# Performance work log

Hardware: AMD Instinct MI355X
Metric: run time of the kernel (lower is better)

The kernel has to match this reference:

```python
import jax, jax.numpy as jnp
import numpy as np

RMS_EPS = 1e-8
Q_EPS = 1e-5

def rms_norm(x):
    # RMSNorm without learnable scale, as in BitNet reference BitLinear
    return x * jax.lax.rsqrt(jnp.mean(x * x, axis=-1, keepdims=True) + RMS_EPS)

def activation_quant(x):
    # per-token absmax int8 quant/dequant
    scale = 127.0 / jnp.clip(jnp.max(jnp.abs(x), axis=-1, keepdims=True), Q_EPS)
    return jnp.clip(jnp.round(x * scale), -128, 127) / scale

def weight_quant(w):
    # ternary absmean quant/dequant
    scale = 1.0 / jnp.clip(jnp.mean(jnp.abs(w)), Q_EPS)
    return jnp.clip(jnp.round(w * scale), -1, 1) / scale

def bitlinear(x, w):
    # forward path of BitLinear: RMSNorm -> quantized matmul (STE is identity in fwd)
    xn = rms_norm(x)
    xq = xn + jax.lax.stop_gradient(activation_quant(xn) - xn)
    wq = w + jax.lax.stop_gradient(weight_quant(w) - w)
    return jnp.einsum('bsh,oh->bso', xq, wq)

def setup_inputs() -> dict:
    key = jax.random.key(0)
    k1, k2, k3 = jax.random.split(key, 3)
    H, I = 2048, 8192  # hidden_size, intermediate_size = 4*H
    x = jax.random.normal(k1, (4, 2048, H), jnp.float32)
    w_gate = jax.random.normal(k2, (2 * I, H), jnp.float32) * 0.02
    w_down = jax.random.normal(k3, (H, I), jnp.float32) * 0.02
    return {"x": x, "w_gate": w_gate, "w_down": w_down}

def reference(x, w_gate, w_down):
    y = bitlinear(x, w_gate)          # [B,S,2I]
    gate, v = jnp.split(y, 2, axis=-1)
    return bitlinear(jax.nn.silu(gate) * v, w_down)  # [B,S,H]
```

## Files before the change

### kernel.cpp

```cpp
#include <hip/hip_runtime.h>


using char8  = __attribute__((ext_vector_type(8))) signed char;
using int4v  = __attribute__((ext_vector_type(4))) int;
using half8  = __attribute__((ext_vector_type(8))) _Float16;

__device__ __forceinline__ void glds16(const void* g, void* l) {
  __builtin_amdgcn_global_load_lds((const __attribute__((address_space(1))) void*)g,
                                   (__attribute__((address_space(3))) void*)l, 16, 0, 0);
}

__global__ __launch_bounds__(256) void reduce_abs_kernel(
    const float4* __restrict__ w, float* __restrict__ partials, int n4) {
  int t = threadIdx.x;
  int gid = blockIdx.x * 256 + t;
  int stride = gridDim.x * 256;
  float s = 0.f;
  for (int i = gid; i < n4; i += stride) {
    float4 u = w[i];
    s += fabsf(u.x) + fabsf(u.y) + fabsf(u.z) + fabsf(u.w);
  }
  __shared__ float sm[256];
  sm[t] = s; __syncthreads();
  for (int off = 128; off > 0; off >>= 1) {
    if (t < off) sm[t] += sm[t + off];
    __syncthreads();
  }
  if (t == 0) partials[blockIdx.x] = sm[0];
}

__global__ __launch_bounds__(256) void finalize_kernel(
    const float* __restrict__ pf, float* __restrict__ scales) {
  __shared__ float sm[256];
  int t = threadIdx.x;
  float s = pf[t] + pf[t + 256] + pf[t + 512] + pf[t + 768];
  sm[t] = s; __syncthreads();
  for (int off = 128; off > 0; off >>= 1) {
    if (t < off) sm[t] += sm[t + off];
    __syncthreads();
  }
  if (t == 0) {
    float c = fmaxf(sm[0] / 33554432.0f, 1e-5f);
    scales[0] = c; scales[2] = 1.0f / c;
  }
  __syncthreads();
  s = pf[1024 + t] + pf[1280 + t] + pf[1536 + t] + pf[1792 + t];
  sm[t] = s; __syncthreads();
  for (int off = 128; off > 0; off >>= 1) {
    if (t < off) sm[t] += sm[t + off];
    __syncthreads();
  }
  if (t == 0) {
    float c = fmaxf(sm[0] / 16777216.0f, 1e-5f);
    scales[1] = c; scales[3] = 1.0f / c;
  }
}

__global__ __launch_bounds__(256) void quant_weight_kernel(
    const float4* __restrict__ w, char8* __restrict__ wq,
    const float* __restrict__ invp, int n8) {
  float inv = *invp;
  int stride = gridDim.x * 256;
  for (int i = blockIdx.x * 256 + threadIdx.x; i < n8; i += stride) {
    float4 a = w[2 * i], b = w[2 * i + 1];
    float v[8] = {a.x, a.y, a.z, a.w, b.x, b.y, b.z, b.w};
    char8 o;
#pragma unroll
    for (int j = 0; j < 8; ++j) {
      float q = rintf(v[j] * inv);
      q = fminf(fmaxf(q, -1.f), 1.f);
      o[j] = (signed char)(int)q;
    }
    wq[i] = o;
  }
}

__global__ __launch_bounds__(256) void act_quant_f32_kernel(
    const float* __restrict__ in, signed char* __restrict__ out,
    float* __restrict__ fscale) {
  const int token = blockIdx.x, t = threadIdx.x;
  const float4* row = (const float4*)(in + (size_t)token * 2048);
  float4 a = row[2 * t], b = row[2 * t + 1];
  float v[8] = {a.x, a.y, a.z, a.w, b.x, b.y, b.z, b.w};
  float ss = 0.f, am = 0.f;
#pragma unroll
  for (int j = 0; j < 8; ++j) { ss += v[j] * v[j]; am = fmaxf(am, fabsf(v[j])); }
  __shared__ float s1[256], s2[256];
  s1[t] = ss; s2[t] = am; __syncthreads();
  for (int off = 128; off > 0; off >>= 1) {
    if (t < off) { s1[t] += s1[t + off]; s2[t] = fmaxf(s2[t], s2[t + off]); }
    __syncthreads();
  }
  float r = 1.0f / sqrtf(s1[0] * (1.0f / 2048.0f) + 1e-8f);
  float f = fmaxf(s2[0] * r, 1e-5f);
  float s = 127.0f / f;
  if (t == 0) fscale[token] = f * (1.0f / 127.0f);
  char8 o;
#pragma unroll
  for (int j = 0; j < 8; ++j) {
    float q = rintf((v[j] * r) * s);
    q = fminf(fmaxf(q, -128.f), 127.f);
    o[j] = (signed char)(int)q;
  }
  ((char8*)(out + (size_t)token * 2048))[t] = o;
}

__global__ __launch_bounds__(256) void act_quant_h_kernel(
    const _Float16* __restrict__ in, signed char* __restrict__ out,
    float* __restrict__ fscale) {
  const int token = blockIdx.x, t = threadIdx.x;
  const half8* row = (const half8*)(in + (size_t)token * 8192);
  float v[32];
  float ss = 0.f, am = 0.f;
#pragma unroll
  for (int c = 0; c < 4; ++c) {
    half8 u = row[c * 256 + t];
#pragma unroll
    for (int j = 0; j < 8; ++j) {
      float f = (float)u[j]; v[c * 8 + j] = f;
      ss += f * f; am = fmaxf(am, fabsf(f));
    }
  }
  __shared__ float s1[256], s2[256];
  s1[t] = ss; s2[t] = am; __syncthreads();
  for (int off = 128; off > 0; off >>= 1) {
    if (t < off) { s1[t] += s1[t + off]; s2[t] = fmaxf(s2[t], s2[t + off]); }
    __syncthreads();
  }
  float r = 1.0f / sqrtf(s1[0] * (1.0f / 8192.0f) + 1e-8f);
  float f = fmaxf(s2[0] * r, 1e-5f);
  float s = 127.0f / f;
  if (t == 0) fscale[token] = f * (1.0f / 127.0f);
#pragma unroll
  for (int c = 0; c < 4; ++c) {
    char8 o;
#pragma unroll
    for (int j = 0; j < 8; ++j) {
      float q = rintf((v[c * 8 + j] * r) * s);
      q = fminf(fmaxf(q, -128.f), 127.f);
      o[j] = (signed char)(int)q;
    }
    ((char8*)(out + (size_t)token * 8192))[c * 256 + t] = o;
  }
}

__global__ __launch_bounds__(256, 2) void gemm1_kernel(
    const signed char* __restrict__ A,
    const signed char* __restrict__ B,
    const float* __restrict__ f1, const float* __restrict__ cgp,
    _Float16* __restrict__ Z) {
  constexpr int K = 2048, I = 8192, NT = K / 64;
  constexpr int BUF = 24576;
  __shared__ __align__(16) signed char Ls[3 * BUF];
  const int t0 = blockIdx.y * 128, n0 = blockIdx.x * 128;
  const int tid = threadIdx.x, w = tid >> 6, l = tid & 63;
  const int wm = (w >> 1) * 64, wn = (w & 1) * 64;
  const int lrow = l & 15, lchunk = (l >> 4) * 16;

  int4v ag[4][4], av[4][4];
#pragma unroll
  for (int i = 0; i < 4; ++i)
#pragma unroll
    for (int j = 0; j < 4; ++j) { ag[i][j] = {0,0,0,0}; av[i][j] = {0,0,0,0}; }

  const signed char* src[6];
  int dst[6];
#pragma unroll
  for (int r = 0; r < 6; ++r) {
    int u = w * 6 + r;
    if (u < 8) {
      src[r] = A + (size_t)(t0 + u * 16 + lrow) * K + lchunk;
      dst[r] = u * 1024;
    } else {
      int v = u - 8;
      int grow = (v < 8) ? (n0 + v * 16 + lrow) : (I + n0 + (v - 8) * 16 + lrow);
      src[r] = B + (size_t)grow * K + lchunk;
      dst[r] = 8192 + v * 1024;
    }
  }

#pragma unroll
  for (int p = 0; p < 3; ++p)
#pragma unroll
    for (int r = 0; r < 6; ++r) glds16(src[r] + p * 64, &Ls[p * BUF + dst[r]]);
  asm volatile("s_waitcnt vmcnt(12)" ::: "memory");
  __builtin_amdgcn_s_barrier();
  __builtin_amdgcn_sched_barrier(0);

  const int aoff = (wm >> 4) * 1024 + l * 16;
  const int goff = 8192 + (wn >> 4) * 1024 + l * 16;
  const int voff = goff + 8 * 1024;

  int curo = 0;
  for (int it = 0; it < NT; ++it) {
    int4v af[4], bg[4], bv[4];
#pragma unroll
    for (int i = 0; i < 4; ++i) af[i] = *(const int4v*)&Ls[curo + aoff + i * 1024];
#pragma unroll
    for (int j = 0; j < 4; ++j) {
      bg[j] = *(const int4v*)&Ls[curo + goff + j * 1024];
      bv[j] = *(const int4v*)&Ls[curo + voff + j * 1024];
    }
    __builtin_amdgcn_s_setprio(1);
#pragma unroll
    for (int i = 0; i < 4; ++i)
#pragma unroll
      for (int j = 0; j < 4; ++j) {
        ag[i][j] = __builtin_amdgcn_mfma_i32_16x16x64_i8(af[i], bg[j], ag[i][j], 0, 0, 0);
        av[i][j] = __builtin_amdgcn_mfma_i32_16x16x64_i8(af[i], bv[j], av[i][j], 0, 0, 0);
      }
    __builtin_amdgcn_s_setprio(0);
    if (it + 3 < NT) {
      __builtin_amdgcn_s_barrier();
      __builtin_amdgcn_sched_barrier(0);
#pragma unroll
      for (int r = 0; r < 6; ++r) glds16(src[r] + (it + 3) * 64, &Ls[curo + dst[r]]);
    }
    if (it < NT - 3)        asm volatile("s_waitcnt vmcnt(12)" ::: "memory");
    else if (it == NT - 3)  asm volatile("s_waitcnt vmcnt(6)" ::: "memory");
    else if (it == NT - 2)  asm volatile("s_waitcnt vmcnt(0)" ::: "memory");
    if (it + 1 < NT) {
      __builtin_amdgcn_s_barrier();
      __builtin_amdgcn_sched_barrier(0);
    }
    curo += BUF; if (curo == 3 * BUF) curo = 0;
  }

  float cg = *cgp;
#pragma unroll
  for (int i = 0; i < 4; ++i)
#pragma unroll
    for (int rr = 0; rr < 4; ++rr) {
      int m = wm + i * 16 + (l >> 4) * 4 + rr;
      float fs = f1[t0 + m] * cg;
#pragma unroll
      for (int j = 0; j < 4; ++j) {
        int n = wn + j * 16 + (l & 15);
        float g = (float)ag[i][j][rr] * fs, vv = (float)av[i][j][rr] * fs;
        float z = g / (1.0f + __expf(-g)) * vv;
        Z[(size_t)(t0 + m) * I + n0 + n] = (_Float16)z;
      }
    }
}

__global__ __launch_bounds__(256, 2) void gemm2_kernel(
    const signed char* __restrict__ A,
    const signed char* __restrict__ B,
    const float* __restrict__ f2, const float* __restrict__ cdp,
    float* __restrict__ out) {
  constexpr int K = 8192, N = 2048, NT = K / 64;
  constexpr int BUF = 24576;
  __shared__ __align__(16) signed char Ls[3 * BUF];
  const int t0 = blockIdx.y * 128, n0 = blockIdx.x * 256;
  const int tid = threadIdx.x, w = tid >> 6, l = tid & 63;
  const int wm = (w >> 1) * 64, wn = (w & 1) * 128;
  const int lrow = l & 15, lchunk = (l >> 4) * 16;

  int4v acc[4][8];
#pragma unroll
  for (int i = 0; i < 4; ++i)
#pragma unroll
    for (int j = 0; j < 8; ++j) acc[i][j] = {0,0,0,0};

  const signed char* src[6];
  int dst[6];
#pragma unroll
  for (int r = 0; r < 6; ++r) {
    int u = w * 6 + r;
    if (u < 8) {
      src[r] = A + (size_t)(t0 + u * 16 + lrow) * K + lchunk;
      dst[r] = u * 1024;
    } else {
      int v = u - 8;
      src[r] = B + (size_t)(n0 + v * 16 + lrow) * K + lchunk;
      dst[r] = 8192 + v * 1024;
    }
  }

#pragma unroll
  for (int p = 0; p < 3; ++p)
#pragma unroll
    for (int r = 0; r < 6; ++r) glds16(src[r] + p * 64, &Ls[p * BUF + dst[r]]);
  asm volatile("s_waitcnt vmcnt(12)" ::: "memory");
  __builtin_amdgcn_s_barrier();
  __builtin_amdgcn_sched_barrier(0);

  const int aoff = (wm >> 4) * 1024 + l * 16;
  const int boff = 8192 + (wn >> 4) * 1024 + l * 16;

  int curo = 0;
  for (int it = 0; it < NT; ++it) {
    int4v af[4], bf[8];
#pragma unroll
    for (int i = 0; i < 4; ++i) af[i] = *(const int4v*)&Ls[curo + aoff + i * 1024];
#pragma unroll
    for (int j = 0; j < 8; ++j) bf[j] = *(const int4v*)&Ls[curo + boff + j * 1024];
    __builtin_amdgcn_s_setprio(1);
#pragma unroll
    for (int i = 0; i < 4; ++i)
#pragma unroll
      for (int j = 0; j < 8; ++j)
        acc[i][j] = __builtin_amdgcn_mfma_i32_16x16x64_i8(af[i], bf[j], acc[i][j], 0, 0, 0);
    __builtin_amdgcn_s_setprio(0);
    if (it + 3 < NT) {
      __builtin_amdgcn_s_barrier();
      __builtin_amdgcn_sched_barrier(0);
#pragma unroll
      for (int r = 0; r < 6; ++r) glds16(src[r] + (it + 3) * 64, &Ls[curo + dst[r]]);
    }
    if (it < NT - 3)        asm volatile("s_waitcnt vmcnt(12)" ::: "memory");
    else if (it == NT - 3)  asm volatile("s_waitcnt vmcnt(6)" ::: "memory");
    else if (it == NT - 2)  asm volatile("s_waitcnt vmcnt(0)" ::: "memory");
    if (it + 1 < NT) {
      __builtin_amdgcn_s_barrier();
      __builtin_amdgcn_sched_barrier(0);
    }
    curo += BUF; if (curo == 3 * BUF) curo = 0;
  }

  float cd = *cdp;
#pragma unroll
  for (int i = 0; i < 4; ++i)
#pragma unroll
    for (int rr = 0; rr < 4; ++rr) {
      int m = wm + i * 16 + (l >> 4) * 4 + rr;
      float fs = f2[t0 + m] * cd;
#pragma unroll
      for (int j = 0; j < 8; ++j) {
        int n = wn + j * 16 + (l & 15);
        out[(size_t)(t0 + m) * N + n0 + n] = (float)acc[i][j][rr] * fs;
      }
    }
}

extern "C" void kernel_launch(void* const* d_in, const int* in_sizes, int n_in,
                              void* d_out, int out_size, void* d_ws, size_t ws_size,
                              hipStream_t stream) {
  const float* x  = (const float*)d_in[0];
  const float* wg = (const float*)d_in[1];
  const float* wd = (const float*)d_in[2];
  float* out = (float*)d_out;

  char* ws = (char*)d_ws;
  signed char* wgq = (signed char*)(ws);
  signed char* wdq = (signed char*)(ws + 33554432);
  signed char* xq  = (signed char*)(ws + 50331648);
  signed char* zq  = (signed char*)(ws + 67108864);
  _Float16*    z   = (_Float16*)  (ws + 134217728);
  float* f1     = (float*)(ws + 268435456);
  float* f2     = (float*)(ws + 268468224);
  float* pf     = (float*)(ws + 268500992);
  float* scales = (float*)(ws + 268509184);

  reduce_abs_kernel<<<1024, 256, 0, stream>>>((const float4*)wg, pf, 8388608);
  reduce_abs_kernel<<<1024, 256, 0, stream>>>((const float4*)wd, pf + 1024, 4194304);
  finalize_kernel<<<1, 256, 0, stream>>>(pf, scales);

  quant_weight_kernel<<<2048, 256, 0, stream>>>((const float4*)wg, (char8*)wgq, scales + 2, 4194304);
  quant_weight_kernel<<<1024, 256, 0, stream>>>((const float4*)wd, (char8*)wdq, scales + 3, 2097152);
  act_quant_f32_kernel<<<8192, 256, 0, stream>>>(x, xq, f1);

  gemm1_kernel<<<dim3(64, 64), 256, 0, stream>>>(xq, wgq, f1, scales, z);

  act_quant_h_kernel<<<8192, 256, 0, stream>>>(z, zq, f2);

  gemm2_kernel<<<dim3(8, 64), 256, 0, stream>>>(zq, wdq, f2, scales + 1, out);
}
```

Measured before the change: 911.1 us.

## Interleave LDS fragment reads, global prefetch and MFMA in sub-phases per K-step

After: 902.8 us. About the same (-0.9%).

```diff
diff --git a/kernel.cpp b/kernel.cpp
--- a/kernel.cpp
+++ b/kernel.cpp
@@ -9,6 +9,8 @@
   __builtin_amdgcn_global_load_lds((const __attribute__((address_space(1))) void*)g,
                                    (__attribute__((address_space(3))) void*)l, 16, 0, 0);
 }
+
+#define SB0() __builtin_amdgcn_sched_barrier(0)
 
 __global__ __launch_bounds__(256) void reduce_abs_kernel(
     const float4* __restrict__ w, float* __restrict__ partials, int n4) {
@@ -180,12 +182,12 @@
   }
 
 #pragma unroll
-  for (int p = 0; p < 3; ++p)
+  for (int p = 0; p < 2; ++p)
 #pragma unroll
     for (int r = 0; r < 6; ++r) glds16(src[r] + p * 64, &Ls[p * BUF + dst[r]]);
-  asm volatile("s_waitcnt vmcnt(12)" ::: "memory");
+  asm volatile("s_waitcnt vmcnt(6)" ::: "memory");
   __builtin_amdgcn_s_barrier();
-  __builtin_amdgcn_sched_barrier(0);
+  SB0();
 
   const int aoff = (wm >> 4) * 1024 + l * 16;
   const int goff = 8192 + (wn >> 4) * 1024 + l * 16;
@@ -193,35 +195,45 @@
 
   int curo = 0;
   for (int it = 0; it < NT; ++it) {
+    int stgo = curo + 2 * BUF; if (stgo >= 3 * BUF) stgo -= 3 * BUF;
+    const bool stg = (it + 2 < NT);
+    const int ko = (it + 2) * 64;
     int4v af[4], bg[4], bv[4];
-#pragma unroll
-    for (int i = 0; i < 4; ++i) af[i] = *(const int4v*)&Ls[curo + aoff + i * 1024];
+
 #pragma unroll
     for (int j = 0; j < 4; ++j) {
+      if (j == 0) {
+#pragma unroll
+        for (int i = 0; i < 4; ++i) af[i] = *(const int4v*)&Ls[curo + aoff + i * 1024];
+      }
       bg[j] = *(const int4v*)&Ls[curo + goff + j * 1024];
       bv[j] = *(const int4v*)&Ls[curo + voff + j * 1024];
-    }
-    __builtin_amdgcn_s_setprio(1);
-#pragma unroll
-    for (int i = 0; i < 4; ++i)
-#pragma unroll
-      for (int j = 0; j < 4; ++j) {
+      if (stg && j < 3) {
+        glds16(src[2 * j] + ko, &Ls[stgo + dst[2 * j]]);
+        glds16(src[2 * j + 1] + ko, &Ls[stgo + dst[2 * j + 1]]);
+      }
+      SB0();
+      __builtin_amdgcn_s_barrier();
+      SB0();
+      __builtin_amdgcn_s_setprio(1);
+#pragma unroll
+      for (int i = 0; i < 4; ++i)
         ag[i][j] = __builtin_amdgcn_mfma_i32_16x16x64_i8(af[i], bg[j], ag[i][j], 0, 0, 0);
+#pragma unroll
+      for (int i = 0; i < 4; ++i)
         av[i][j] = __builtin_amdgcn_mfma_i32_16x16x64_i8(af[i], bv[j], av[i][j], 0, 0, 0);
-      }
-    __builtin_amdgcn_s_setprio(0);
-    if (it + 3 < NT) {
-      __builtin_amdgcn_s_barrier();
-      __builtin_amdgcn_sched_barrier(0);
-#pragma unroll
-      for (int r = 0; r < 6; ++r) glds16(src[r] + (it + 3) * 64, &Ls[curo + dst[r]]);
-    }
-    if (it < NT - 3)        asm volatile("s_waitcnt vmcnt(12)" ::: "memory");
-    else if (it == NT - 3)  asm volatile("s_waitcnt vmcnt(6)" ::: "memory");
-    else if (it == NT - 2)  asm volatile("s_waitcnt vmcnt(0)" ::: "memory");
+      __builtin_amdgcn_s_setprio(0);
+      SB0();
+      if (j < 3) {
+        __builtin_amdgcn_s_barrier();
+        SB0();
+      }
+    }
+    if (it < NT - 2)       asm volatile("s_waitcnt vmcnt(6)" ::: "memory");
+    else if (it == NT - 2) asm volatile("s_waitcnt vmcnt(0)" ::: "memory");
     if (it + 1 < NT) {
       __builtin_amdgcn_s_barrier();
-      __builtin_amdgcn_sched_barrier(0);
+      SB0();
     }
     curo += BUF; if (curo == 3 * BUF) curo = 0;
   }
@@ -278,42 +290,57 @@
   }
 
 #pragma unroll
-  for (int p = 0; p < 3; ++p)
+  for (int p = 0; p < 2; ++p)
 #pragma unroll
     for (int r = 0; r < 6; ++r) glds16(src[r] + p * 64, &Ls[p * BUF + dst[r]]);
-  asm volatile("s_waitcnt vmcnt(12)" ::: "memory");
+  asm volatile("s_waitcnt vmcnt(6)" ::: "memory");
   __builtin_amdgcn_s_barrier();
-  __builtin_amdgcn_sched_barrier(0);
+  SB0();
 
   const int aoff = (wm >> 4) * 1024 + l * 16;
   const int boff = 8192 + (wn >> 4) * 1024 + l * 16;
 
   int curo = 0;
   for (int it = 0; it < NT; ++it) {
+    int stgo = curo + 2 * BUF; if (stgo >= 3 * BUF) stgo -= 3 * BUF;
+    const bool stg = (it + 2 < NT);
+    const int ko = (it + 2) * 64;
     int4v af[4], bf[8];
-#pragma unroll
-    for (int i = 0; i < 4; ++i) af[i] = *(const int4v*)&Ls[curo + aoff + i * 1024];
-#pragma unroll
-    for (int j = 0; j < 8; ++j) bf[j] = *(const int4v*)&Ls[curo + boff + j * 1024];
-    __builtin_amdgcn_s_setprio(1);
-#pragma unroll
-    for (int i = 0; i < 4; ++i)
-#pragma unroll
-      for (int j = 0; j < 8; ++j)
-        acc[i][j] = __builtin_amdgcn_mfma_i32_16x16x64_i8(af[i], bf[j], acc[i][j], 0, 0, 0);
-    __builtin_amdgcn_s_setprio(0);
-    if (it + 3 < NT) {
+
+#pragma unroll
+    for (int p = 0; p < 4; ++p) {
+      if (p == 0) {
+#pragma unroll
+        for (int i = 0; i < 4; ++i) af[i] = *(const int4v*)&Ls[curo + aoff + i * 1024];
+      }
+      bf[2 * p]     = *(const int4v*)&Ls[curo + boff + (2 * p) * 1024];
+      bf[2 * p + 1] = *(const int4v*)&Ls[curo + boff + (2 * p + 1) * 1024];
+      if (stg && p < 3) {
+        glds16(src[2 * p] + ko, &Ls[stgo + dst[2 * p]]);
+        glds16(src[2 * p + 1] + ko, &Ls[stgo + dst[2 * p + 1]]);
+      }
+      SB0();
       __builtin_amdgcn_s_barrier();
-      __builtin_amdgcn_sched_barrier(0);
-#pragma unroll
-      for (int r = 0; r < 6; ++r) glds16(src[r] + (it + 3) * 64, &Ls[curo + dst[r]]);
-    }
-    if (it < NT - 3)        asm volatile("s_waitcnt vmcnt(12)" ::: "memory");
-    else if (it == NT - 3)  asm volatile("s_waitcnt vmcnt(6)" ::: "memory");
-    else if (it == NT - 2)  asm volatile("s_waitcnt vmcnt(0)" ::: "memory");
+      SB0();
+      __builtin_amdgcn_s_setprio(1);
+#pragma unroll
+      for (int i = 0; i < 4; ++i)
+        acc[i][2 * p] = __builtin_amdgcn_mfma_i32_16x16x64_i8(af[i], bf[2 * p], acc[i][2 * p], 0, 0, 0);
+#pragma unroll
+      for (int i = 0; i < 4; ++i)
+        acc[i][2 * p + 1] = __builtin_amdgcn_mfma_i32_16x16x64_i8(af[i], bf[2 * p + 1], acc[i][2 * p + 1], 0, 0, 0);
+      __builtin_amdgcn_s_setprio(0);
+      SB0();
+      if (p < 3) {
+        __builtin_amdgcn_s_barrier();
+        SB0();
+      }
+    }
+    if (it < NT - 2)       asm volatile("s_waitcnt vmcnt(6)" ::: "memory");
+    else if (it == NT - 2) asm volatile("s_waitcnt vmcnt(0)" ::: "memory");
     if (it + 1 < NT) {
       __builtin_amdgcn_s_barrier();
-      __builtin_amdgcn_sched_barrier(0);
+      SB0();
     }
     curo += BUF; if (curo == 3 * BUF) curo = 0;
   }
```
